# Optimization experiments

Hardware: AMD Instinct MI355X
Metric: run time of the kernel (lower is better)

The kernel has to match this reference:

```python
import jax, jax.numpy as jnp
import numpy as np

B, N, D, A = 4, 2048, 1024, 256


def setup_inputs() -> dict:
    key = jax.random.key(0)
    k1, k2, k3, k4, k5 = jax.random.split(key, 5)
    s = 1.0 / np.sqrt(D)
    return {
        "inputs": jax.random.normal(k1, (B, N, D), dtype=jnp.float32),
        "attention_mask": jnp.zeros((B, 1, N), dtype=jnp.float32),
        "Wq": jax.random.normal(k2, (D, A), dtype=jnp.float32) * s,
        "bq": jax.random.normal(k3, (A,), dtype=jnp.float32) * 0.01,
        "Wk": jax.random.normal(k4, (D, A), dtype=jnp.float32) * s,
        "bk": jax.random.normal(k5, (A,), dtype=jnp.float32) * 0.01,
    }


def reference(inputs, attention_mask, Wq, bq, Wk, bk):
    # q, k: [B, N, A]; v = inputs: [B, N, D]
    q = jnp.einsum('bnd,da->bna', inputs, Wq) + bq
    k = jnp.einsum('bnd,da->bna', inputs, Wk) + bk
    # unscaled scores, faithful to source (no 1/sqrt(d))
    scores = jnp.einsum('bna,bma->bnm', q, k) + attention_mask  # [B, N, N]
    probs = jax.nn.softmax(scores, axis=-1)
    # dropout is identity in eval mode
    context = jnp.einsum('bnm,bmd->bnd', probs, inputs)  # [B, N, D]
    return context
```

## Files before the change

### kernel.cpp

```cpp
#include <hip/hip_runtime.h>
#include <hip/hip_bf16.h>


#define BB 4
#define NN 2048
#define DD 1024
#define AA 256

using bf16x8 = __attribute__((ext_vector_type(8))) __bf16;
using f32x4  = __attribute__((ext_vector_type(4))) float;

#define MFMA(a, b, c) __builtin_amdgcn_mfma_f32_16x16x32_bf16(a, b, c, 0, 0, 0)

#define VMCNT(n) asm volatile("s_waitcnt vmcnt(" #n ")" ::: "memory")
#define CFENCE() asm volatile("" ::: "memory")
#define BARRIER() __builtin_amdgcn_s_barrier()

static __device__ __forceinline__ unsigned short f2bf(float x) {
    union { float f; unsigned int u; } c; c.f = x;
    unsigned int u = c.u;
    u += 0x7fffu + ((u >> 16) & 1u);
    return (unsigned short)(u >> 16);
}
static __device__ __forceinline__ float bf2f(unsigned short h) {
    union { unsigned int u; float f; } c; c.u = ((unsigned int)h) << 16;
    return c.f;
}

template<int SLOTS>
static __device__ __forceinline__ int swz(int r) {
    return (SLOTS == 4) ? ((r >> 1) & 3) : (r & 7);
}

template<int BK>
static __device__ __forceinline__ void stage_tile(const unsigned short* __restrict__ g,
                                                  int pitch, unsigned short* lds, int t) {
    constexpr int SLOTS = BK / 8;
    constexpr int ISSUES = (128 * SLOTS) / 256;
#pragma unroll
    for (int i = 0; i < ISSUES; ++i) {
        int tt = t + i * 256;
        int row = tt / SLOTS;
        int slot = (tt % SLOTS) ^ swz<SLOTS>(row);
        const char* src = (const char*)(g + (size_t)row * pitch) + slot * 16;
        __builtin_amdgcn_global_load_lds((const unsigned int*)src,
                                         (unsigned int*)((char*)lds + (size_t)tt * 16),
                                         16, 0, 0);
    }
}

template<int BK>
static __device__ __forceinline__ bf16x8 ldsfrag(const unsigned short* lds, int row,
                                                 int ks, int lane) {
    constexpr int SLOTS = BK / 8;
    int r = row + (lane & 15);
    int slot = (ks * 4 + (lane >> 4)) ^ swz<SLOTS>(r);
    return *reinterpret_cast<const bf16x8*>((const char*)lds + (size_t)r * (BK * 2) + slot * 16);
}

__global__ __launch_bounds__(256) void k_prep(const float* __restrict__ X,
                                              unsigned short* __restrict__ Xh,
                                              unsigned short* __restrict__ Xl,
                                              unsigned short* __restrict__ XT) {
    __shared__ unsigned short tile[64][65];
    int t = threadIdx.x;
    int n0 = blockIdx.x * 64, d0 = blockIdx.y * 64;
    const float* Xb = X + (size_t)blockIdx.z * NN * DD;
    unsigned short* Xhb = Xh + (size_t)blockIdx.z * NN * DD;
    unsigned short* Xlb = Xl + (size_t)blockIdx.z * NN * DD;
    unsigned short* XTb = XT + (size_t)blockIdx.z * DD * NN;
    int r = t >> 4, c4 = (t & 15) * 4;
#pragma unroll
    for (int i = 0; i < 4; ++i) {
        int row = r + 16 * i;
        float4 v = *reinterpret_cast<const float4*>(Xb + (size_t)(n0 + row) * DD + d0 + c4);
        ushort4 h, l;
        h.x = f2bf(v.x); l.x = f2bf(v.x - bf2f(h.x));
        h.y = f2bf(v.y); l.y = f2bf(v.y - bf2f(h.y));
        h.z = f2bf(v.z); l.z = f2bf(v.z - bf2f(h.z));
        h.w = f2bf(v.w); l.w = f2bf(v.w - bf2f(h.w));
        *reinterpret_cast<ushort4*>(Xhb + (size_t)(n0 + row) * DD + d0 + c4) = h;
        *reinterpret_cast<ushort4*>(Xlb + (size_t)(n0 + row) * DD + d0 + c4) = l;
        tile[c4 + 0][row] = h.x;
        tile[c4 + 1][row] = h.y;
        tile[c4 + 2][row] = h.z;
        tile[c4 + 3][row] = h.w;
    }
    __syncthreads();
    int j = t & 63, i4 = t >> 6;
#pragma unroll
    for (int jj = i4; jj < 64; jj += 4)
        XTb[(size_t)(d0 + jj) * NN + n0 + j] = tile[jj][j];
}

__global__ __launch_bounds__(256) void k_wsplit(const float* __restrict__ W,
                                                unsigned short* __restrict__ WTh,
                                                unsigned short* __restrict__ WTl) {
    int idx = blockIdx.x * 256 + threadIdx.x;
    int a = idx >> 10;
    int d = idx & (DD - 1);
    float w = W[(size_t)d * AA + a];
    unsigned short hi = f2bf(w);
    WTh[idx] = hi;
    WTl[idx] = f2bf(w - bf2f(hi));
}

__global__ __launch_bounds__(256) void k_proj(const unsigned short* __restrict__ Xh,
                                              const unsigned short* __restrict__ Xl,
                                              const unsigned short* __restrict__ WqTh,
                                              const unsigned short* __restrict__ WqTl,
                                              const unsigned short* __restrict__ WkTh,
                                              const unsigned short* __restrict__ WkTl,
                                              const float* __restrict__ bq,
                                              const float* __restrict__ bk,
                                              unsigned short* __restrict__ Qh,
                                              unsigned short* __restrict__ Ql,
                                              unsigned short* __restrict__ Kh,
                                              unsigned short* __restrict__ Kl) {
    __shared__ unsigned short ldsAh[2][128 * 32], ldsAl[2][128 * 32];
    __shared__ unsigned short ldsBh[2][128 * 32], ldsBl[2][128 * 32];
    int t = threadIdx.x, lane = t & 63, wave = t >> 6;
    int row0 = blockIdx.x * 128;
    int which = blockIdx.y >> 1;
    int col0 = (blockIdx.y & 1) * 128;
    const unsigned short* BTh = which ? WkTh : WqTh;
    const unsigned short* BTl = which ? WkTl : WqTl;
    const float* bias = which ? bk : bq;
    unsigned short* Oh = which ? Kh : Qh;
    unsigned short* Ol = which ? Kl : Ql;
    const unsigned short* Abase_h = Xh + (size_t)row0 * DD;
    const unsigned short* Abase_l = Xl + (size_t)row0 * DD;
    const unsigned short* Bbase_h = BTh + (size_t)col0 * DD;
    const unsigned short* Bbase_l = BTl + (size_t)col0 * DD;
    int wr = (wave >> 1) * 64, wc = (wave & 1) * 64;
    f32x4 acc[4][4] = {};
    stage_tile<32>(Abase_h, DD, ldsAh[0], t);
    stage_tile<32>(Abase_l, DD, ldsAl[0], t);
    stage_tile<32>(Bbase_h, DD, ldsBh[0], t);
    stage_tile<32>(Bbase_l, DD, ldsBl[0], t);
    constexpr int NT = DD / 32;
    for (int tt = 0; tt < NT; ++tt) {
        int cur = tt & 1;
        CFENCE();
        BARRIER();
        if (tt + 1 < NT) {
            int k0 = (tt + 1) * 32;
            stage_tile<32>(Abase_h + k0, DD, ldsAh[cur ^ 1], t);
            stage_tile<32>(Abase_l + k0, DD, ldsAl[cur ^ 1], t);
            stage_tile<32>(Bbase_h + k0, DD, ldsBh[cur ^ 1], t);
            stage_tile<32>(Bbase_l + k0, DD, ldsBl[cur ^ 1], t);
            VMCNT(8);
        } else {
            VMCNT(0);
        }
        BARRIER();
        CFENCE();
        bf16x8 ah[4], al[4], bh[4], bl[4];
#pragma unroll
        for (int f = 0; f < 4; ++f) {
            ah[f] = ldsfrag<32>(ldsAh[cur], wr + f * 16, 0, lane);
            al[f] = ldsfrag<32>(ldsAl[cur], wr + f * 16, 0, lane);
            bh[f] = ldsfrag<32>(ldsBh[cur], wc + f * 16, 0, lane);
            bl[f] = ldsfrag<32>(ldsBl[cur], wc + f * 16, 0, lane);
        }
#pragma unroll
        for (int m = 0; m < 4; ++m)
#pragma unroll
            for (int n = 0; n < 4; ++n) {
                acc[m][n] = MFMA(ah[m], bh[n], acc[m][n]);
                acc[m][n] = MFMA(ah[m], bl[n], acc[m][n]);
                acc[m][n] = MFMA(al[m], bh[n], acc[m][n]);
            }
    }
    int r4 = (lane >> 4) << 2, cl = lane & 15;
#pragma unroll
    for (int m = 0; m < 4; ++m)
#pragma unroll
        for (int n = 0; n < 4; ++n) {
            int col = col0 + wc + n * 16 + cl;
            float bv = bias[col];
#pragma unroll
            for (int r = 0; r < 4; ++r) {
                int row = row0 + wr + m * 16 + r4 + r;
                float v = acc[m][n][r] + bv;
                unsigned short hi = f2bf(v);
                size_t o = (size_t)row * AA + col;
                Oh[o] = hi;
                Ol[o] = f2bf(v - bf2f(hi));
            }
        }
}

__global__ __launch_bounds__(256) void k_scores(const unsigned short* __restrict__ Qh,
                                                const unsigned short* __restrict__ Ql,
                                                const unsigned short* __restrict__ Kh,
                                                const unsigned short* __restrict__ Kl,
                                                float* __restrict__ S) {
    __shared__ unsigned short ldsAh[2][128 * 32], ldsAl[2][128 * 32];
    __shared__ unsigned short ldsBh[2][128 * 32], ldsBl[2][128 * 32];
    int t = threadIdx.x, lane = t & 63, wave = t >> 6;
    int b = blockIdx.z;
    int nrow0 = blockIdx.x * 128;
    int mcol0 = blockIdx.y * 128;
    const unsigned short* Qhb = Qh + (size_t)(b * NN + nrow0) * AA;
    const unsigned short* Qlb = Ql + (size_t)(b * NN + nrow0) * AA;
    const unsigned short* Khb = Kh + (size_t)(b * NN + mcol0) * AA;
    const unsigned short* Klb = Kl + (size_t)(b * NN + mcol0) * AA;
    int wr = (wave >> 1) * 64, wc = (wave & 1) * 64;
    f32x4 acc[4][4] = {};
    stage_tile<32>(Qhb, AA, ldsAh[0], t);
    stage_tile<32>(Qlb, AA, ldsAl[0], t);
    stage_tile<32>(Khb, AA, ldsBh[0], t);
    stage_tile<32>(Klb, AA, ldsBl[0], t);
    constexpr int NT = AA / 32;
    for (int tt = 0; tt < NT; ++tt) {
        int cur = tt & 1;
        CFENCE();
        BARRIER();
        if (tt + 1 < NT) {
            int k0 = (tt + 1) * 32;
            stage_tile<32>(Qhb + k0, AA, ldsAh[cur ^ 1], t);
            stage_tile<32>(Qlb + k0, AA, ldsAl[cur ^ 1], t);
            stage_tile<32>(Khb + k0, AA, ldsBh[cur ^ 1], t);
            stage_tile<32>(Klb + k0, AA, ldsBl[cur ^ 1], t);
            VMCNT(8);
        } else {
            VMCNT(0);
        }
        BARRIER();
        CFENCE();
        bf16x8 ah[4], al[4], bh[4], bl[4];
#pragma unroll
        for (int f = 0; f < 4; ++f) {
            ah[f] = ldsfrag<32>(ldsAh[cur], wr + f * 16, 0, lane);
            al[f] = ldsfrag<32>(ldsAl[cur], wr + f * 16, 0, lane);
            bh[f] = ldsfrag<32>(ldsBh[cur], wc + f * 16, 0, lane);
            bl[f] = ldsfrag<32>(ldsBl[cur], wc + f * 16, 0, lane);
        }
#pragma unroll
        for (int m = 0; m < 4; ++m)
#pragma unroll
            for (int n = 0; n < 4; ++n) {
                acc[m][n] = MFMA(ah[m], bh[n], acc[m][n]);
                acc[m][n] = MFMA(ah[m], bl[n], acc[m][n]);
                acc[m][n] = MFMA(al[m], bh[n], acc[m][n]);
            }
    }
    int r4 = (lane >> 4) << 2, cl = lane & 15;
#pragma unroll
    for (int m = 0; m < 4; ++m)
#pragma unroll
        for (int n = 0; n < 4; ++n) {
#pragma unroll
            for (int r = 0; r < 4; ++r) {
                int nrow = nrow0 + wr + m * 16 + r4 + r;
                int mcol = mcol0 + wc + n * 16 + cl;
                S[((size_t)(b * NN + nrow)) * NN + mcol] = acc[m][n][r];
            }
        }
}

__global__ __launch_bounds__(256) void k_softmax(float* __restrict__ S,
                                                 const float* __restrict__ mask) {
    int row = blockIdx.x;
    int b = row >> 11;
    float* srow = S + (size_t)row * NN;
    const float* mrow = mask + (size_t)b * NN;
    int t = threadIdx.x;
    float v[8];
    float mx = -3.0e38f;
#pragma unroll
    for (int i = 0; i < 8; ++i) {
        int m = t + i * 256;
        v[i] = srow[m] + mrow[m];
        mx = fmaxf(mx, v[i]);
    }
#pragma unroll
    for (int off = 32; off; off >>= 1) mx = fmaxf(mx, __shfl_xor(mx, off));
    __shared__ float redm[4], reds[4];
    int lane = t & 63, wave = t >> 6;
    if (lane == 0) redm[wave] = mx;
    __syncthreads();
    mx = fmaxf(fmaxf(redm[0], redm[1]), fmaxf(redm[2], redm[3]));
    float s = 0.f;
#pragma unroll
    for (int i = 0; i < 8; ++i) { v[i] = __expf(v[i] - mx); s += v[i]; }
#pragma unroll
    for (int off = 32; off; off >>= 1) s += __shfl_xor(s, off);
    if (lane == 0) reds[wave] = s;
    __syncthreads();
    s = reds[0] + reds[1] + reds[2] + reds[3];
    float inv = 1.0f / s;
    unsigned short* prow = (unsigned short*)srow;
#pragma unroll
    for (int i = 0; i < 8; ++i) {
        int m = t + i * 256;
        prow[m] = f2bf(v[i] * inv);
    }
}

__global__ __launch_bounds__(256) void k_pv(const float* __restrict__ Sbuf,
                                            const unsigned short* __restrict__ XT,
                                            float* __restrict__ Out) {
    __shared__ unsigned short ldsA[2][128 * 64], ldsB[2][128 * 64];
    int t = threadIdx.x, lane = t & 63, wave = t >> 6;
    int b = blockIdx.z;
    int nrow0 = blockIdx.x * 128;
    int d0    = blockIdx.y * 128;
    const unsigned short* P = (const unsigned short*)Sbuf;
    const unsigned short* Pb = P + (size_t)(b * NN + nrow0) * (NN * 2);
    const unsigned short* XTb = XT + (size_t)b * DD * NN + (size_t)d0 * NN;
    int wr = (wave >> 1) * 64, wc = (wave & 1) * 64;
    f32x4 acc[4][4] = {};
    stage_tile<64>(Pb, NN * 2, ldsA[0], t);
    stage_tile<64>(XTb, NN, ldsB[0], t);
    constexpr int NT = NN / 64;
    for (int tt = 0; tt < NT; ++tt) {
        int cur = tt & 1;
        CFENCE();
        BARRIER();
        if (tt + 1 < NT) {
            int m0 = (tt + 1) * 64;
            stage_tile<64>(Pb + m0, NN * 2, ldsA[cur ^ 1], t);
            stage_tile<64>(XTb + m0, NN, ldsB[cur ^ 1], t);
            VMCNT(8);
        } else {
            VMCNT(0);
        }
        BARRIER();
        CFENCE();
        bf16x8 pa[2][4], vb[2][4];
#pragma unroll
        for (int ks = 0; ks < 2; ++ks)
#pragma unroll
            for (int f = 0; f < 4; ++f) {
                pa[ks][f] = ldsfrag<64>(ldsA[cur], wr + f * 16, ks, lane);
                vb[ks][f] = ldsfrag<64>(ldsB[cur], wc + f * 16, ks, lane);
            }
#pragma unroll
        for (int ks = 0; ks < 2; ++ks)
#pragma unroll
            for (int m = 0; m < 4; ++m)
#pragma unroll
                for (int n = 0; n < 4; ++n)
                    acc[m][n] = MFMA(pa[ks][m], vb[ks][n], acc[m][n]);
    }
    int r4 = (lane >> 4) << 2, cl = lane & 15;
#pragma unroll
    for (int m = 0; m < 4; ++m)
#pragma unroll
        for (int n = 0; n < 4; ++n) {
#pragma unroll
            for (int r = 0; r < 4; ++r) {
                int row = b * NN + nrow0 + wr + m * 16 + r4 + r;
                int dc = d0 + wc + n * 16 + cl;
                Out[(size_t)row * DD + dc] = acc[m][n][r];
            }
        }
}

extern "C" void kernel_launch(void* const* d_in, const int* in_sizes, int n_in,
                              void* d_out, int out_size, void* d_ws, size_t ws_size,
                              hipStream_t stream) {
    const float* X    = (const float*)d_in[0];
    const float* mask = (const float*)d_in[1];
    const float* Wq   = (const float*)d_in[2];
    const float* bq   = (const float*)d_in[3];
    const float* Wk   = (const float*)d_in[4];
    const float* bk   = (const float*)d_in[5];
    float* Out = (float*)d_out;

    unsigned short* Xh   = (unsigned short*)d_ws;
    unsigned short* Xl   = Xh + (size_t)BB * NN * DD;
    unsigned short* XT   = Xl + (size_t)BB * NN * DD;
    unsigned short* WqTh = XT + (size_t)BB * NN * DD;
    unsigned short* WqTl = WqTh + (size_t)AA * DD;
    unsigned short* WkTh = WqTl + (size_t)AA * DD;
    unsigned short* WkTl = WkTh + (size_t)AA * DD;
    unsigned short* Qh   = WkTl + (size_t)AA * DD;
    unsigned short* Ql   = Qh + (size_t)BB * NN * AA;
    unsigned short* Kh   = Ql + (size_t)BB * NN * AA;
    unsigned short* Kl   = Kh + (size_t)BB * NN * AA;
    float* S = (float*)(Kl + (size_t)BB * NN * AA);

    k_prep<<<dim3(NN / 64, DD / 64, BB), 256, 0, stream>>>(X, Xh, Xl, XT);
    k_wsplit<<<dim3((AA * DD) / 256), 256, 0, stream>>>(Wq, WqTh, WqTl);
    k_wsplit<<<dim3((AA * DD) / 256), 256, 0, stream>>>(Wk, WkTh, WkTl);

    k_proj<<<dim3((BB * NN) / 128, 4), 256, 0, stream>>>(Xh, Xl, WqTh, WqTl, WkTh, WkTl,
                                                         bq, bk, Qh, Ql, Kh, Kl);

    k_scores<<<dim3(NN / 128, NN / 128, BB), 256, 0, stream>>>(Qh, Ql, Kh, Kl, S);
    k_softmax<<<dim3(BB * NN), 256, 0, stream>>>(S, mask);
    k_pv<<<dim3(NN / 128, DD / 128, BB), 256, 0, stream>>>(S, XT, Out);
}
```

Baseline: 161.9 us.

## Retile projection, vectorize softmax, triple-buffer PV GEMM with 512-thread blocks

The projection kernel now uses 64-row tiles, doubling its grid for better occupancy, and both projection and score MFMA loops are wrapped in raised wave priority. Softmax loads and stores through float4 and ushort4 vectors. The PV kernel is rebuilt with 512 threads, 128x256 tiles in dynamic LDS, three-stage buffering with prefetch interleaved between MFMA sub-steps, and a remapped block order for cache locality. Together these aim to raise MFMA utilization and hide memory latency, in exchange for heavy LDS use (144KB) that limits PV residency.

```diff
diff --git a/kernel.cpp b/kernel.cpp
--- a/kernel.cpp
+++ b/kernel.cpp
@@ -32,14 +32,13 @@
     return (SLOTS == 4) ? ((r >> 1) & 3) : (r & 7);
 }
 
-template<int BK>
-static __device__ __forceinline__ void stage_tile(const unsigned short* __restrict__ g,
+template<int ROWS, int BK, int THREADS, int I0, int I1>
+static __device__ __forceinline__ void stage_part(const unsigned short* __restrict__ g,
                                                   int pitch, unsigned short* lds, int t) {
     constexpr int SLOTS = BK / 8;
-    constexpr int ISSUES = (128 * SLOTS) / 256;
-#pragma unroll
-    for (int i = 0; i < ISSUES; ++i) {
-        int tt = t + i * 256;
+#pragma unroll
+    for (int i = I0; i < I1; ++i) {
+        int tt = t + i * THREADS;
         int row = tt / SLOTS;
         int slot = (tt % SLOTS) ^ swz<SLOTS>(row);
         const char* src = (const char*)(g + (size_t)row * pitch) + slot * 16;
@@ -117,10 +116,10 @@
                                               unsigned short* __restrict__ Ql,
                                               unsigned short* __restrict__ Kh,
                                               unsigned short* __restrict__ Kl) {
-    __shared__ unsigned short ldsAh[2][128 * 32], ldsAl[2][128 * 32];
+    __shared__ unsigned short ldsAh[2][64 * 32], ldsAl[2][64 * 32];
     __shared__ unsigned short ldsBh[2][128 * 32], ldsBl[2][128 * 32];
     int t = threadIdx.x, lane = t & 63, wave = t >> 6;
-    int row0 = blockIdx.x * 128;
+    int row0 = blockIdx.x * 64;
     int which = blockIdx.y >> 1;
     int col0 = (blockIdx.y & 1) * 128;
     const unsigned short* BTh = which ? WkTh : WqTh;
@@ -132,12 +131,12 @@
     const unsigned short* Abase_l = Xl + (size_t)row0 * DD;
     const unsigned short* Bbase_h = BTh + (size_t)col0 * DD;
     const unsigned short* Bbase_l = BTl + (size_t)col0 * DD;
-    int wr = (wave >> 1) * 64, wc = (wave & 1) * 64;
-    f32x4 acc[4][4] = {};
-    stage_tile<32>(Abase_h, DD, ldsAh[0], t);
-    stage_tile<32>(Abase_l, DD, ldsAl[0], t);
-    stage_tile<32>(Bbase_h, DD, ldsBh[0], t);
-    stage_tile<32>(Bbase_l, DD, ldsBl[0], t);
+    int wc = wave * 32;
+    f32x4 acc[4][2] = {};
+    stage_part<64, 32, 256, 0, 1>(Abase_h, DD, ldsAh[0], t);
+    stage_part<64, 32, 256, 0, 1>(Abase_l, DD, ldsAl[0], t);
+    stage_part<128, 32, 256, 0, 2>(Bbase_h, DD, ldsBh[0], t);
+    stage_part<128, 32, 256, 0, 2>(Bbase_l, DD, ldsBl[0], t);
     constexpr int NT = DD / 32;
     for (int tt = 0; tt < NT; ++tt) {
         int cur = tt & 1;
@@ -145,43 +144,48 @@
         BARRIER();
         if (tt + 1 < NT) {
             int k0 = (tt + 1) * 32;
-            stage_tile<32>(Abase_h + k0, DD, ldsAh[cur ^ 1], t);
-            stage_tile<32>(Abase_l + k0, DD, ldsAl[cur ^ 1], t);
-            stage_tile<32>(Bbase_h + k0, DD, ldsBh[cur ^ 1], t);
-            stage_tile<32>(Bbase_l + k0, DD, ldsBl[cur ^ 1], t);
-            VMCNT(8);
+            stage_part<64, 32, 256, 0, 1>(Abase_h + k0, DD, ldsAh[cur ^ 1], t);
+            stage_part<64, 32, 256, 0, 1>(Abase_l + k0, DD, ldsAl[cur ^ 1], t);
+            stage_part<128, 32, 256, 0, 2>(Bbase_h + k0, DD, ldsBh[cur ^ 1], t);
+            stage_part<128, 32, 256, 0, 2>(Bbase_l + k0, DD, ldsBl[cur ^ 1], t);
+            VMCNT(6);
         } else {
             VMCNT(0);
         }
         BARRIER();
         CFENCE();
-        bf16x8 ah[4], al[4], bh[4], bl[4];
+        bf16x8 ah[4], al[4], bh[2], bl[2];
 #pragma unroll
         for (int f = 0; f < 4; ++f) {
-            ah[f] = ldsfrag<32>(ldsAh[cur], wr + f * 16, 0, lane);
-            al[f] = ldsfrag<32>(ldsAl[cur], wr + f * 16, 0, lane);
-            bh[f] = ldsfrag<32>(ldsBh[cur], wc + f * 16, 0, lane);
-            bl[f] = ldsfrag<32>(ldsBl[cur], wc + f * 16, 0, lane);
-        }
+            ah[f] = ldsfrag<32>(ldsAh[cur], f * 16, 0, lane);
+            al[f] = ldsfrag<32>(ldsAl[cur], f * 16, 0, lane);
+        }
+#pragma unroll
+        for (int n = 0; n < 2; ++n) {
+            bh[n] = ldsfrag<32>(ldsBh[cur], wc + n * 16, 0, lane);
+            bl[n] = ldsfrag<32>(ldsBl[cur], wc + n * 16, 0, lane);
+        }
+        __builtin_amdgcn_s_setprio(1);
 #pragma unroll
         for (int m = 0; m < 4; ++m)
 #pragma unroll
-            for (int n = 0; n < 4; ++n) {
+            for (int n = 0; n < 2; ++n) {
                 acc[m][n] = MFMA(ah[m], bh[n], acc[m][n]);
                 acc[m][n] = MFMA(ah[m], bl[n], acc[m][n]);
                 acc[m][n] = MFMA(al[m], bh[n], acc[m][n]);
             }
+        __builtin_amdgcn_s_setprio(0);
     }
     int r4 = (lane >> 4) << 2, cl = lane & 15;
 #pragma unroll
     for (int m = 0; m < 4; ++m)
 #pragma unroll
-        for (int n = 0; n < 4; ++n) {
+        for (int n = 0; n < 2; ++n) {
             int col = col0 + wc + n * 16 + cl;
             float bv = bias[col];
 #pragma unroll
             for (int r = 0; r < 4; ++r) {
-                int row = row0 + wr + m * 16 + r4 + r;
+                int row = row0 + m * 16 + r4 + r;
                 float v = acc[m][n][r] + bv;
                 unsigned short hi = f2bf(v);
                 size_t o = (size_t)row * AA + col;
@@ -208,10 +212,10 @@
     const unsigned short* Klb = Kl + (size_t)(b * NN + mcol0) * AA;
     int wr = (wave >> 1) * 64, wc = (wave & 1) * 64;
     f32x4 acc[4][4] = {};
-    stage_tile<32>(Qhb, AA, ldsAh[0], t);
-    stage_tile<32>(Qlb, AA, ldsAl[0], t);
-    stage_tile<32>(Khb, AA, ldsBh[0], t);
-    stage_tile<32>(Klb, AA, ldsBl[0], t);
+    stage_part<128, 32, 256, 0, 2>(Qhb, AA, ldsAh[0], t);
+    stage_part<128, 32, 256, 0, 2>(Qlb, AA, ldsAl[0], t);
+    stage_part<128, 32, 256, 0, 2>(Khb, AA, ldsBh[0], t);
+    stage_part<128, 32, 256, 0, 2>(Klb, AA, ldsBl[0], t);
     constexpr int NT = AA / 32;
     for (int tt = 0; tt < NT; ++tt) {
         int cur = tt & 1;
@@ -219,10 +223,10 @@
         BARRIER();
         if (tt + 1 < NT) {
             int k0 = (tt + 1) * 32;
-            stage_tile<32>(Qhb + k0, AA, ldsAh[cur ^ 1], t);
-            stage_tile<32>(Qlb + k0, AA, ldsAl[cur ^ 1], t);
-            stage_tile<32>(Khb + k0, AA, ldsBh[cur ^ 1], t);
-            stage_tile<32>(Klb + k0, AA, ldsBl[cur ^ 1], t);
+            stage_part<128, 32, 256, 0, 2>(Qhb + k0, AA, ldsAh[cur ^ 1], t);
+            stage_part<128, 32, 256, 0, 2>(Qlb + k0, AA, ldsAl[cur ^ 1], t);
+            stage_part<128, 32, 256, 0, 2>(Khb + k0, AA, ldsBh[cur ^ 1], t);
+            stage_part<128, 32, 256, 0, 2>(Klb + k0, AA, ldsBl[cur ^ 1], t);
             VMCNT(8);
         } else {
             VMCNT(0);
@@ -237,6 +241,7 @@
             bh[f] = ldsfrag<32>(ldsBh[cur], wc + f * 16, 0, lane);
             bl[f] = ldsfrag<32>(ldsBl[cur], wc + f * 16, 0, lane);
         }
+        __builtin_amdgcn_s_setprio(1);
 #pragma unroll
         for (int m = 0; m < 4; ++m)
 #pragma unroll
@@ -245,6 +250,7 @@
                 acc[m][n] = MFMA(ah[m], bl[n], acc[m][n]);
                 acc[m][n] = MFMA(al[m], bh[n], acc[m][n]);
             }
+        __builtin_amdgcn_s_setprio(0);
     }
     int r4 = (lane >> 4) << 2, cl = lane & 15;
 #pragma unroll
@@ -265,16 +271,17 @@
     int row = blockIdx.x;
     int b = row >> 11;
     float* srow = S + (size_t)row * NN;
-    const float* mrow = mask + (size_t)b * NN;
+    const float4* S4 = (const float4*)srow;
+    const float4* M4 = (const float4*)(mask + (size_t)b * NN);
     int t = threadIdx.x;
+    float4 a0 = S4[t], a1 = S4[t + 256];
+    float4 m0 = M4[t], m1 = M4[t + 256];
     float v[8];
-    float mx = -3.0e38f;
-#pragma unroll
-    for (int i = 0; i < 8; ++i) {
-        int m = t + i * 256;
-        v[i] = srow[m] + mrow[m];
-        mx = fmaxf(mx, v[i]);
-    }
+    v[0] = a0.x + m0.x; v[1] = a0.y + m0.y; v[2] = a0.z + m0.z; v[3] = a0.w + m0.w;
+    v[4] = a1.x + m1.x; v[5] = a1.y + m1.y; v[6] = a1.z + m1.z; v[7] = a1.w + m1.w;
+    float mx = v[0];
+#pragma unroll
+    for (int i = 1; i < 8; ++i) mx = fmaxf(mx, v[i]);
 #pragma unroll
     for (int off = 32; off; off >>= 1) mx = fmaxf(mx, __shfl_xor(mx, off));
     __shared__ float redm[4], reds[4];
@@ -291,70 +298,92 @@
     __syncthreads();
     s = reds[0] + reds[1] + reds[2] + reds[3];
     float inv = 1.0f / s;
-    unsigned short* prow = (unsigned short*)srow;
-#pragma unroll
-    for (int i = 0; i < 8; ++i) {
-        int m = t + i * 256;
-        prow[m] = f2bf(v[i] * inv);
-    }
-}
-
-__global__ __launch_bounds__(256) void k_pv(const float* __restrict__ Sbuf,
-                                            const unsigned short* __restrict__ XT,
-                                            float* __restrict__ Out) {
-    __shared__ unsigned short ldsA[2][128 * 64], ldsB[2][128 * 64];
+    ushort4 w0, w1;
+    w0.x = f2bf(v[0] * inv); w0.y = f2bf(v[1] * inv);
+    w0.z = f2bf(v[2] * inv); w0.w = f2bf(v[3] * inv);
+    w1.x = f2bf(v[4] * inv); w1.y = f2bf(v[5] * inv);
+    w1.z = f2bf(v[6] * inv); w1.w = f2bf(v[7] * inv);
+    ushort4* prow4 = (ushort4*)srow;
+    prow4[t] = w0;
+    prow4[t + 256] = w1;
+}
+
+__global__ __launch_bounds__(512, 2) void k_pv(const float* __restrict__ Sbuf,
+                                               const unsigned short* __restrict__ XT,
+                                               float* __restrict__ Out) {
+    extern __shared__ unsigned short dyn[];
     int t = threadIdx.x, lane = t & 63, wave = t >> 6;
-    int b = blockIdx.z;
-    int nrow0 = blockIdx.x * 128;
-    int d0    = blockIdx.y * 128;
-    const unsigned short* P = (const unsigned short*)Sbuf;
-    const unsigned short* Pb = P + (size_t)(b * NN + nrow0) * (NN * 2);
+    int wm = wave >> 2, wn = wave & 3;
+    int bid = blockIdx.x + 16 * (blockIdx.y + 4 * blockIdx.z);
+    int sbid = (bid & 7) * 32 + (bid >> 3);
+    int bx = sbid & 15;
+    int by = (sbid >> 4) & 3;
+    int b = sbid >> 6;
+    int nrow0 = bx * 128, d0 = by * 256;
+    const unsigned short* Pb = (const unsigned short*)Sbuf + (size_t)(b * NN + nrow0) * (NN * 2);
     const unsigned short* XTb = XT + (size_t)b * DD * NN + (size_t)d0 * NN;
-    int wr = (wave >> 1) * 64, wc = (wave & 1) * 64;
     f32x4 acc[4][4] = {};
-    stage_tile<64>(Pb, NN * 2, ldsA[0], t);
-    stage_tile<64>(XTb, NN, ldsB[0], t);
+    stage_part<128, 64, 512, 0, 2>(Pb, NN * 2, dyn, t);
+    stage_part<256, 64, 512, 0, 4>(XTb, NN, dyn + 24576, t);
+    stage_part<128, 64, 512, 0, 2>(Pb + 64, NN * 2, dyn + 8192, t);
+    stage_part<256, 64, 512, 0, 4>(XTb + 64, NN, dyn + 24576 + 16384, t);
     constexpr int NT = NN / 64;
-    for (int tt = 0; tt < NT; ++tt) {
-        int cur = tt & 1;
+    int cur = 0;
+    for (int kt = 0; kt < NT; ++kt) {
+        int st = (cur >= 1) ? cur - 1 : 2;
+        const unsigned short* An = Pb + (kt + 2) * 64;
+        const unsigned short* Bn = XTb + (kt + 2) * 64;
+        bool pf = (kt + 2 < NT);
         CFENCE();
         BARRIER();
-        if (tt + 1 < NT) {
-            int m0 = (tt + 1) * 64;
-            stage_tile<64>(Pb + m0, NN * 2, ldsA[cur ^ 1], t);
-            stage_tile<64>(XTb + m0, NN, ldsB[cur ^ 1], t);
-            VMCNT(8);
-        } else {
-            VMCNT(0);
-        }
-        BARRIER();
-        CFENCE();
-        bf16x8 pa[2][4], vb[2][4];
-#pragma unroll
-        for (int ks = 0; ks < 2; ++ks)
-#pragma unroll
-            for (int f = 0; f < 4; ++f) {
-                pa[ks][f] = ldsfrag<64>(ldsA[cur], wr + f * 16, ks, lane);
-                vb[ks][f] = ldsfrag<64>(ldsB[cur], wc + f * 16, ks, lane);
-            }
-#pragma unroll
-        for (int ks = 0; ks < 2; ++ks)
-#pragma unroll
-            for (int m = 0; m < 4; ++m)
-#pragma unroll
-                for (int n = 0; n < 4; ++n)
-                    acc[m][n] = MFMA(pa[ks][m], vb[ks][n], acc[m][n]);
+        if (kt == NT - 1) { VMCNT(0); } else { VMCNT(6); }
+        CFENCE();
+        const unsigned short* A = dyn + cur * 8192;
+        const unsigned short* Bt = dyn + 24576 + cur * 16384;
+        unsigned short* Ast = dyn + st * 8192;
+        unsigned short* Bst = dyn + 24576 + st * 16384;
+#pragma unroll
+        for (int p = 0; p < 4; ++p) {
+            int mq = p >> 1, nq = p & 1;
+            if (pf) {
+                if (p == 0)      stage_part<128, 64, 512, 0, 2>(An, NN * 2, Ast, t);
+                else if (p == 1) stage_part<256, 64, 512, 0, 2>(Bn, NN, Bst, t);
+                else if (p == 2) stage_part<256, 64, 512, 2, 4>(Bn, NN, Bst, t);
+            }
+            bf16x8 pa[2][2], vb[2][2];
+#pragma unroll
+            for (int m = 0; m < 2; ++m)
+#pragma unroll
+                for (int ks = 0; ks < 2; ++ks)
+                    pa[m][ks] = ldsfrag<64>(A, wm * 64 + mq * 32 + m * 16, ks, lane);
+#pragma unroll
+            for (int n = 0; n < 2; ++n)
+#pragma unroll
+                for (int ks = 0; ks < 2; ++ks)
+                    vb[n][ks] = ldsfrag<64>(Bt, wn * 64 + nq * 32 + n * 16, ks, lane);
+            __builtin_amdgcn_s_setprio(1);
+#pragma unroll
+            for (int ks = 0; ks < 2; ++ks)
+#pragma unroll
+                for (int m = 0; m < 2; ++m)
+#pragma unroll
+                    for (int n = 0; n < 2; ++n)
+                        acc[mq * 2 + m][nq * 2 + n] =
+                            MFMA(pa[m][ks], vb[n][ks], acc[mq * 2 + m][nq * 2 + n]);
+            __builtin_amdgcn_s_setprio(0);
+        }
+        cur = (cur == 2) ? 0 : cur + 1;
     }
     int r4 = (lane >> 4) << 2, cl = lane & 15;
 #pragma unroll
-    for (int m = 0; m < 4; ++m)
-#pragma unroll
-        for (int n = 0; n < 4; ++n) {
+    for (int mi = 0; mi < 4; ++mi)
+#pragma unroll
+        for (int ni = 0; ni < 4; ++ni) {
 #pragma unroll
             for (int r = 0; r < 4; ++r) {
-                int row = b * NN + nrow0 + wr + m * 16 + r4 + r;
-                int dc = d0 + wc + n * 16 + cl;
-                Out[(size_t)row * DD + dc] = acc[m][n][r];
+                int row = b * NN + nrow0 + wm * 64 + mi * 16 + r4 + r;
+                int dc = d0 + wn * 64 + ni * 16 + cl;
+                Out[(size_t)row * DD + dc] = acc[mi][ni][r];
             }
         }
 }
@@ -383,14 +412,17 @@
     unsigned short* Kl   = Kh + (size_t)BB * NN * AA;
     float* S = (float*)(Kl + (size_t)BB * NN * AA);
 
+    hipFuncSetAttribute((const void*)k_pv,
+                        hipFuncAttributeMaxDynamicSharedMemorySize, 147456);
+
     k_prep<<<dim3(NN / 64, DD / 64, BB), 256, 0, stream>>>(X, Xh, Xl, XT);
     k_wsplit<<<dim3((AA * DD) / 256), 256, 0, stream>>>(Wq, WqTh, WqTl);
     k_wsplit<<<dim3((AA * DD) / 256), 256, 0, stream>>>(Wk, WkTh, WkTl);
 
-    k_proj<<<dim3((BB * NN) / 128, 4), 256, 0, stream>>>(Xh, Xl, WqTh, WqTl, WkTh, WkTl,
-                                                         bq, bk, Qh, Ql, Kh, Kl);
+    k_proj<<<dim3((BB * NN) / 64, 4), 256, 0, stream>>>(Xh, Xl, WqTh, WqTl, WkTh, WkTl,
+                                                        bq, bk, Qh, Ql, Kh, Kl);
 
     k_scores<<<dim3(NN / 128, NN / 128, BB), 256, 0, stream>>>(Qh, Ql, Kh, Kl, S);
     k_softmax<<<dim3(BB * NN), 256, 0, stream>>>(S, mask);
-    k_pv<<<dim3(NN / 128, DD / 128, BB), 256, 0, stream>>>(S, XT, Out);
-}
+    k_pv<<<dim3(16, 4, BB), 512, 147456, stream>>>(S, XT, Out);
+}
```

Result: faster. 153.4 us (-5.3%).
